# Optimization experiments

Measured on AMD Instinct MI355X. Metric: run time of the kernel, lower is better.

## Reference

```python
import jax, jax.numpy as jnp
import numpy as np

N, C, H, W = 8, 256, 64, 64
Q_REDUCE, K_REDUCE, V_REDUCE = 8, 8, 1


def setup_inputs() -> dict:
    key = jax.random.key(0)
    ks = jax.random.split(key, 6)
    Cq, Ck, Cv = C // Q_REDUCE, C // K_REDUCE, C // V_REDUCE
    s = 0.02
    x = jax.random.normal(ks[0], (N, C, H, W), dtype=jnp.float32)
    Wq = jax.random.normal(ks[1], (Cq, C), dtype=jnp.float32) * s
    Wk = jax.random.normal(ks[2], (Ck, C), dtype=jnp.float32) * s
    Wv = jax.random.normal(ks[3], (Cv, C), dtype=jnp.float32) * s
    Wo = jax.random.normal(ks[4], (C, Cv), dtype=jnp.float32) * s
    gamma = jax.random.normal(ks[5], (), dtype=jnp.float32)  # trained scalar (init 0.0 in torch)
    return {"x": x, "Wq": Wq, "Wk": Wk, "Wv": Wv, "Wo": Wo, "gamma": gamma}


def reference(x, Wq, Wk, Wv, Wo, gamma):
    n, c, h, w = x.shape
    xf = x.reshape(n, c, h * w)                      # [N, C, HW]
    q = jnp.einsum('qc,ncl->nql', Wq, xf)            # [N, Cq, HW] (1x1 conv)
    k = jnp.einsum('kc,ncl->nkl', Wk, xf)            # [N, Ck, HW]
    v = jnp.einsum('vc,ncl->nvl', Wv, xf)            # [N, Cv, HW]
    e = jnp.einsum('nci,ncj->nij', q, k)             # [N, HW, HW], unscaled energies
    a = jax.nn.softmax(e, axis=-1)                   # softmax over keys j
    o = jnp.einsum('nvi,nij->nvj', v, a)             # [N, Cv, HW]  (o = bmm(v, a))
    o = o.reshape(n, -1, w, h)                       # faithful: view(N,-1,W,H)
    out = jnp.einsum('ov,nvhw->nohw', Wo, o)         # output 1x1 conv
    return gamma * out
```

## Files before the change

### kernel.cpp

```cpp
#include <hip/hip_runtime.h>
#include <hip/hip_bf16.h>

#define NB 8
#define CIN 256
#define LL 4096
#define CQ 32
#define CV 256

typedef __attribute__((ext_vector_type(8))) short bf16x8;
typedef __attribute__((ext_vector_type(4))) float f32x4;

__device__ __forceinline__ unsigned short f2bf(float f) {
    union { __hip_bfloat16 h; unsigned short u; } c;
    c.h = __float2bfloat16(f);
    return c.u;
}
__device__ __forceinline__ unsigned int f2bf2(float a, float b) {
    union { __hip_bfloat162 h; unsigned int u; } c;
    float2 f; f.x = a; f.y = b;
    c.h = __float22bfloat162_rn(f);
    return c.u;
}

__global__ __launch_bounds__(256) void k_wcast(
    const float* __restrict__ Wq, const float* __restrict__ Wk,
    const float* __restrict__ Wv, const float* __restrict__ Wo,
    unsigned short* __restrict__ Wb, unsigned short* __restrict__ Wob)
{
    const float LOG2E = 1.4426950408889634f;
    const int row = blockIdx.x, t = threadIdx.x;
    if (row < 320) {
        float val;
        if (row < 32)      val = Wq[row * 256 + t] * LOG2E;
        else if (row < 64) val = Wk[(row - 32) * 256 + t];
        else               val = Wv[(row - 64) * 256 + t];
        Wb[row * 256 + t] = f2bf(val);
    } else {
        const int r2 = row - 320;
        Wob[r2 * 256 + t] = f2bf(Wo[r2 * 256 + t]);
    }
}

__global__ __launch_bounds__(512) void k_qkv3(
    const float* __restrict__ x, const unsigned short* __restrict__ Wb,
    unsigned short* __restrict__ qkt, unsigned short* __restrict__ v)
{
    __shared__ unsigned short xlds[64][264];
    __shared__ unsigned short tr[64][72];
    const int n = blockIdx.y, l0 = blockIdx.x * 64, t = threadIdx.x;
    const int w = t >> 6, lane = t & 63, lid = lane & 15, quad = lane >> 4;

    #pragma unroll
    for (int part = 0; part < 4; part++) {
        const int cbase = part * 64 + w * 8;
        float tmp[8];
        #pragma unroll
        for (int cc = 0; cc < 8; cc++)
            tmp[cc] = x[((size_t)n * CIN + cbase + cc) * LL + l0 + lane];
        bf16x8 s;
        #pragma unroll
        for (int cc = 0; cc < 8; cc++) s[cc] = (short)f2bf(tmp[cc]);
        *(bf16x8*)&xlds[lane][cbase] = s;
    }
    __syncthreads();

    const f32x4 fzero = {0.f, 0.f, 0.f, 0.f};
    f32x4 acc[3][4];
    #pragma unroll
    for (int mt = 0; mt < 3; mt++)
        #pragma unroll
        for (int nt = 0; nt < 4; nt++) acc[mt][nt] = fzero;

    for (int k0 = 0; k0 < 256; k0 += 32) {
        bf16x8 bx[4];
        #pragma unroll
        for (int nt = 0; nt < 4; nt++)
            bx[nt] = *(const bf16x8*)&xlds[nt * 16 + lid][k0 + quad * 8];
        #pragma unroll
        for (int vt = 0; vt < 2; vt++) {
            const bf16x8 wa = *(const bf16x8*)&Wb[(64 + w * 32 + vt * 16 + lid) * 256 + k0 + quad * 8];
            #pragma unroll
            for (int nt = 0; nt < 4; nt++)
                acc[vt][nt] = __builtin_amdgcn_mfma_f32_16x16x32_bf16(wa, bx[nt], acc[vt][nt], 0, 0, 0);
        }
        if (w < 4) {
            const bf16x8 wa = *(const bf16x8*)&Wb[(w * 16 + lid) * 256 + k0 + quad * 8];
            #pragma unroll
            for (int nt = 0; nt < 4; nt++)
                acc[2][nt] = __builtin_amdgcn_mfma_f32_16x16x32_bf16(wa, bx[nt], acc[2][nt], 0, 0, 0);
        }
    }
    #pragma unroll
    for (int vt = 0; vt < 2; vt++)
        #pragma unroll
        for (int nt = 0; nt < 4; nt++)
            #pragma unroll
            for (int reg = 0; reg < 4; reg++) {
                const int vr = w * 32 + vt * 16 + quad * 4 + reg;
                v[((size_t)n * CV + vr) * LL + l0 + nt * 16 + lid] = f2bf(acc[vt][nt][reg]);
            }
    if (w < 4) {
        #pragma unroll
        for (int nt = 0; nt < 4; nt++)
            #pragma unroll
            for (int reg = 0; reg < 4; reg++)
                tr[nt * 16 + lid][w * 16 + quad * 4 + reg] = f2bf(acc[2][nt][reg]);
    }
    __syncthreads();
    {
        const int l = t >> 3, c = (t & 7) * 8;
        *(uint4*)&qkt[((size_t)n * LL + l0 + l) * 64 + c] = *(const uint4*)&tr[l][c];
    }
}

__global__ __launch_bounds__(512) void k_rowsum3(
    const unsigned short* __restrict__ qkt, float* __restrict__ lns)
{
    __shared__ float red[64];
    const int n = blockIdx.y, i0 = blockIdx.x * 64, t = threadIdx.x;
    const int w = t >> 6, lid = t & 15, quad = (t & 63) >> 4;
    if (t < 64) red[t] = 0.f;
    __syncthreads();

    bf16x8 aq[4];
    #pragma unroll
    for (int mt = 0; mt < 4; mt++)
        aq[mt] = *(const bf16x8*)&qkt[((size_t)n * LL + i0 + mt * 16 + lid) * 64 + quad * 8];

    const f32x4 fzero = {0.f, 0.f, 0.f, 0.f};
    float sums[4][4];
    #pragma unroll
    for (int mt = 0; mt < 4; mt++)
        #pragma unroll
        for (int reg = 0; reg < 4; reg++) sums[mt][reg] = 0.f;

    for (int jt = 0; jt < 8; jt++) {
        const int j0 = jt * 512 + w * 64;
        bf16x8 bk[4];
        #pragma unroll
        for (int nt = 0; nt < 4; nt++)
            bk[nt] = *(const bf16x8*)&qkt[((size_t)n * LL + j0 + nt * 16 + lid) * 64 + 32 + quad * 8];
        #pragma unroll
        for (int mt = 0; mt < 4; mt++)
            #pragma unroll
            for (int nt = 0; nt < 4; nt++) {
                f32x4 e = __builtin_amdgcn_mfma_f32_16x16x32_bf16(aq[mt], bk[nt], fzero, 0, 0, 0);
                sums[mt][0] += __builtin_amdgcn_exp2f(e[0]);
                sums[mt][1] += __builtin_amdgcn_exp2f(e[1]);
                sums[mt][2] += __builtin_amdgcn_exp2f(e[2]);
                sums[mt][3] += __builtin_amdgcn_exp2f(e[3]);
            }
    }
    #pragma unroll
    for (int mt = 0; mt < 4; mt++)
        #pragma unroll
        for (int reg = 0; reg < 4; reg++) {
            float s = sums[mt][reg];
            s += __shfl_xor(s, 1); s += __shfl_xor(s, 2);
            s += __shfl_xor(s, 4); s += __shfl_xor(s, 8);
            if (lid == 0) atomicAdd(&red[mt * 16 + quad * 4 + reg], s);
        }
    __syncthreads();
    if (t < 64) lns[(size_t)n * LL + i0 + t] = -__builtin_log2f(red[t]);
}

__device__ __forceinline__ void write_p(unsigned short (*pl)[128], const f32x4* e,
                                        int w, int lid, int quad, int xkey)
{
    const int chunk = (2 * w + (quad >> 1)) ^ xkey;
    #pragma unroll
    for (int nt = 0; nt < 4; nt++) {
        uint2 d;
        d.x = f2bf2(__builtin_amdgcn_exp2f(e[nt][0]), __builtin_amdgcn_exp2f(e[nt][1]));
        d.y = f2bf2(__builtin_amdgcn_exp2f(e[nt][2]), __builtin_amdgcn_exp2f(e[nt][3]));
        *(uint2*)&pl[nt * 16 + lid][chunk * 8 + (quad & 1) * 4] = d;
    }
}

__global__ __launch_bounds__(512, 4) void k_attn6(
    const unsigned short* __restrict__ qkt, const unsigned short* __restrict__ v,
    const float* __restrict__ lns, const unsigned short* __restrict__ Wob,
    const float* __restrict__ gp, float* __restrict__ out)
{
    __shared__ unsigned short lraw[64 * 264];
    unsigned short (*plds)[64][128] = (unsigned short (*)[64][128])lraw;
    unsigned short (*olds)[264] = (unsigned short (*)[264])lraw;

    const int bid = blockIdx.x;
    const int n = bid & 7, j0 = (bid >> 3) * 64, t = threadIdx.x;
    const int w = t >> 6, lane = t & 63, lid = lane & 15, quad = lane >> 4;
    const int xkey = lid & 7;

    const unsigned short* qrow = qkt + ((size_t)n * LL + w * 16 + lid) * 64 + quad * 8;
    const float* lrow = lns + (size_t)n * LL + w * 16 + quad * 4;
    const unsigned short* vrow = v + ((size_t)n * CV + w * 32 + lid) * LL + quad * 8;

    bf16x8 bk[4];
    #pragma unroll
    for (int nt = 0; nt < 4; nt++)
        bk[nt] = *(const bf16x8*)&qkt[((size_t)n * LL + j0 + nt * 16 + lid) * 64 + 32 + quad * 8];

    const f32x4 fzero = {0.f, 0.f, 0.f, 0.f};
    f32x4 acc[2][4];
    #pragma unroll
    for (int mt = 0; mt < 2; mt++)
        #pragma unroll
        for (int nt = 0; nt < 4; nt++) acc[mt][nt] = fzero;

    bf16x8 aq = *(const bf16x8*)qrow;
    f32x4 lnsC = *(const f32x4*)lrow;
    {
        f32x4 e[4];
        #pragma unroll
        for (int nt = 0; nt < 4; nt++)
            e[nt] = __builtin_amdgcn_mfma_f32_16x16x32_bf16(aq, bk[nt], lnsC, 0, 0, 0);
        aq = *(const bf16x8*)(qrow + (size_t)128 * 64);
        lnsC = *(const f32x4*)(lrow + 128);
        write_p(plds[0], e, w, lid, quad, xkey);
    }
    bf16x8 av[8];
    #pragma unroll
    for (int mt = 0; mt < 2; mt++)
        #pragma unroll
        for (int h = 0; h < 4; h++)
            av[mt * 4 + h] = *(const bf16x8*)(vrow + (size_t)mt * 16 * LL + h * 32);
    __syncthreads();

    for (int ic = 0; ic < 31; ic++) {
        const int cur = ic & 1;
        const size_t i0 = (size_t)ic * 128;
        f32x4 e2[4];
        #pragma unroll
        for (int nt = 0; nt < 4; nt++)
            e2[nt] = __builtin_amdgcn_mfma_f32_16x16x32_bf16(aq, bk[nt], lnsC, 0, 0, 0);
        const size_t ipf = (ic < 30) ? (i0 + 256) : i0;
        aq = *(const bf16x8*)(qrow + ipf * 64);
        lnsC = *(const f32x4*)(lrow + ipf);
        write_p(plds[cur ^ 1], e2, w, lid, quad, xkey);
        #pragma unroll
        for (int h = 0; h < 4; h++) {
            bf16x8 bp[4];
            #pragma unroll
            for (int nt = 0; nt < 4; nt++)
                bp[nt] = *(const bf16x8*)&plds[cur][nt * 16 + lid][((4 * h + quad) ^ xkey) * 8];
            #pragma unroll
            for (int mt = 0; mt < 2; mt++)
                #pragma unroll
                for (int nt = 0; nt < 4; nt++)
                    acc[mt][nt] = __builtin_amdgcn_mfma_f32_16x16x32_bf16(av[mt * 4 + h], bp[nt], acc[mt][nt], 0, 0, 0);
            #pragma unroll
            for (int mt = 0; mt < 2; mt++)
                av[mt * 4 + h] = *(const bf16x8*)(vrow + (size_t)mt * 16 * LL + (i0 + 128) + h * 32);
        }
        __syncthreads();
    }
    #pragma unroll
    for (int h = 0; h < 4; h++) {
        bf16x8 bp[4];
        #pragma unroll
        for (int nt = 0; nt < 4; nt++)
            bp[nt] = *(const bf16x8*)&plds[1][nt * 16 + lid][((4 * h + quad) ^ xkey) * 8];
        #pragma unroll
        for (int mt = 0; mt < 2; mt++)
            #pragma unroll
            for (int nt = 0; nt < 4; nt++)
                acc[mt][nt] = __builtin_amdgcn_mfma_f32_16x16x32_bf16(av[mt * 4 + h], bp[nt], acc[mt][nt], 0, 0, 0);
    }
    __syncthreads();

    #pragma unroll
    for (int mt = 0; mt < 2; mt++)
        #pragma unroll
        for (int nt = 0; nt < 4; nt++) {
            ushort4 s;
            s.x = f2bf(acc[mt][nt][0]); s.y = f2bf(acc[mt][nt][1]);
            s.z = f2bf(acc[mt][nt][2]); s.w = f2bf(acc[mt][nt][3]);
            *(ushort4*)&olds[nt * 16 + lid][w * 32 + mt * 16 + quad * 4] = s;
        }
    __syncthreads();
    f32x4 oacc[2][4];
    #pragma unroll
    for (int mt = 0; mt < 2; mt++)
        #pragma unroll
        for (int nt = 0; nt < 4; nt++) oacc[mt][nt] = fzero;
    for (int k0 = 0; k0 < 256; k0 += 32) {
        bf16x8 bo[4];
        #pragma unroll
        for (int nt = 0; nt < 4; nt++)
            bo[nt] = *(const bf16x8*)&olds[nt * 16 + lid][k0 + quad * 8];
        #pragma unroll
        for (int mt = 0; mt < 2; mt++) {
            const bf16x8 wa = *(const bf16x8*)&Wob[(w * 32 + mt * 16 + lid) * 256 + k0 + quad * 8];
            #pragma unroll
            for (int nt = 0; nt < 4; nt++)
                oacc[mt][nt] = __builtin_amdgcn_mfma_f32_16x16x32_bf16(wa, bo[nt], oacc[mt][nt], 0, 0, 0);
        }
    }
    const float g = *gp;
    #pragma unroll
    for (int mt = 0; mt < 2; mt++)
        #pragma unroll
        for (int nt = 0; nt < 4; nt++)
            #pragma unroll
            for (int reg = 0; reg < 4; reg++) {
                const int r = w * 32 + mt * 16 + quad * 4 + reg;
                out[((size_t)n * CIN + r) * LL + j0 + nt * 16 + lid] = g * oacc[mt][nt][reg];
            }
}

extern "C" void kernel_launch(void* const* d_in, const int* in_sizes, int n_in,
                              void* d_out, int out_size, void* d_ws, size_t ws_size,
                              hipStream_t stream) {
    const float* x     = (const float*)d_in[0];
    const float* Wq    = (const float*)d_in[1];
    const float* Wk    = (const float*)d_in[2];
    const float* Wv    = (const float*)d_in[3];
    const float* Wo    = (const float*)d_in[4];
    const float* gamma = (const float*)d_in[5];

    unsigned short* qkt = (unsigned short*)d_ws;
    unsigned short* v   = qkt + (size_t)NB * LL * 64;
    unsigned short* Wb  = v + (size_t)NB * CV * LL;
    unsigned short* Wob = Wb + 320 * 256;
    float* lns          = (float*)(Wob + 256 * 256);
    float* out = (float*)d_out;

    k_wcast  <<<dim3(576),   256, 0, stream>>>(Wq, Wk, Wv, Wo, Wb, Wob);
    k_qkv3   <<<dim3(64, 8), 512, 0, stream>>>(x, Wb, qkt, v);
    k_rowsum3<<<dim3(64, 8), 512, 0, stream>>>(qkt, lns);
    k_attn6  <<<dim3(512),   512, 0, stream>>>(qkt, v, lns, Wob, gamma, out);
}
```

Baseline: 265.6 us.

## Split attention PV across two key-halves with wider per-wave channel tiles

Restructures the P·V stage so each wave owns 64 value channels (4 M-tiles) for half of each 128-key chunk, with two wave groups splitting keys and reducing partial outputs through shared memory at the end. The P tile is stored in a fragment-ready layout so each wave reads its B operand with a single contiguous load per lane instead of swizzled row reads. The intent is more MFMA reuse per P/V register load and less LDS traffic per MFMA. In exchange it raises accumulator register pressure (16 tiles instead of 8), adds a cross-group reduction that rounds the partial sum to bf16 before adding, and uses more shared memory.

```diff
diff --git a/kernel.cpp b/kernel.cpp
--- a/kernel.cpp
+++ b/kernel.cpp
@@ -15,11 +15,8 @@
     c.h = __float2bfloat16(f);
     return c.u;
 }
-__device__ __forceinline__ unsigned int f2bf2(float a, float b) {
-    union { __hip_bfloat162 h; unsigned int u; } c;
-    float2 f; f.x = a; f.y = b;
-    c.h = __float22bfloat162_rn(f);
-    return c.u;
+__device__ __forceinline__ float bf2f(unsigned short h) {
+    return __uint_as_float(((unsigned)h) << 16);
 }
 
 __global__ __launch_bounds__(256) void k_wcast(
@@ -164,36 +161,26 @@
     if (t < 64) lns[(size_t)n * LL + i0 + t] = -__builtin_log2f(red[t]);
 }
 
-__device__ __forceinline__ void write_p(unsigned short (*pl)[128], const f32x4* e,
-                                        int w, int lid, int quad, int xkey)
-{
-    const int chunk = (2 * w + (quad >> 1)) ^ xkey;
-    #pragma unroll
-    for (int nt = 0; nt < 4; nt++) {
-        uint2 d;
-        d.x = f2bf2(__builtin_amdgcn_exp2f(e[nt][0]), __builtin_amdgcn_exp2f(e[nt][1]));
-        d.y = f2bf2(__builtin_amdgcn_exp2f(e[nt][2]), __builtin_amdgcn_exp2f(e[nt][3]));
-        *(uint2*)&pl[nt * 16 + lid][chunk * 8 + (quad & 1) * 4] = d;
-    }
-}
-
-__global__ __launch_bounds__(512, 4) void k_attn6(
+__global__ __launch_bounds__(512, 4) void k_attn7(
     const unsigned short* __restrict__ qkt, const unsigned short* __restrict__ v,
     const float* __restrict__ lns, const unsigned short* __restrict__ Wob,
     const float* __restrict__ gp, float* __restrict__ out)
 {
-    __shared__ unsigned short lraw[64 * 264];
-    unsigned short (*plds)[64][128] = (unsigned short (*)[64][128])lraw;
-    unsigned short (*olds)[264] = (unsigned short (*)[264])lraw;
+    __shared__ unsigned short pbuf[2][4][4][64][8];
+    __shared__ unsigned short olds[64][264];
+    unsigned short* cbuf = &pbuf[0][0][0][0][0];
 
     const int bid = blockIdx.x;
     const int n = bid & 7, j0 = (bid >> 3) * 64, t = threadIdx.x;
     const int w = t >> 6, lane = t & 63, lid = lane & 15, quad = lane >> 4;
-    const int xkey = lid & 7;
+    const int g = w >> 2, wl = w & 3;
+    const int kbw = w >> 1;
+    const int qr = (w & 1) * 2 + (quad >> 1);
+    const int e0 = (quad & 1) * 4;
 
     const unsigned short* qrow = qkt + ((size_t)n * LL + w * 16 + lid) * 64 + quad * 8;
     const float* lrow = lns + (size_t)n * LL + w * 16 + quad * 4;
-    const unsigned short* vrow = v + ((size_t)n * CV + w * 32 + lid) * LL + quad * 8;
+    const unsigned short* vbase = v + ((size_t)n * CV + wl * 64 + lid) * LL + g * 64 + quad * 8;
 
     bf16x8 bk[4];
     #pragma unroll
@@ -201,9 +188,9 @@
         bk[nt] = *(const bf16x8*)&qkt[((size_t)n * LL + j0 + nt * 16 + lid) * 64 + 32 + quad * 8];
 
     const f32x4 fzero = {0.f, 0.f, 0.f, 0.f};
-    f32x4 acc[2][4];
-    #pragma unroll
-    for (int mt = 0; mt < 2; mt++)
+    f32x4 acc[4][4];
+    #pragma unroll
+    for (int mt = 0; mt < 4; mt++)
         #pragma unroll
         for (int nt = 0; nt < 4; nt++) acc[mt][nt] = fzero;
 
@@ -216,14 +203,20 @@
             e[nt] = __builtin_amdgcn_mfma_f32_16x16x32_bf16(aq, bk[nt], lnsC, 0, 0, 0);
         aq = *(const bf16x8*)(qrow + (size_t)128 * 64);
         lnsC = *(const f32x4*)(lrow + 128);
-        write_p(plds[0], e, w, lid, quad, xkey);
-    }
-    bf16x8 av[8];
-    #pragma unroll
-    for (int mt = 0; mt < 2; mt++)
-        #pragma unroll
-        for (int h = 0; h < 4; h++)
-            av[mt * 4 + h] = *(const bf16x8*)(vrow + (size_t)mt * 16 * LL + h * 32);
+        #pragma unroll
+        for (int nt = 0; nt < 4; nt++) {
+            ushort4 s;
+            s.x = f2bf(__builtin_amdgcn_exp2f(e[nt][0]));
+            s.y = f2bf(__builtin_amdgcn_exp2f(e[nt][1]));
+            s.z = f2bf(__builtin_amdgcn_exp2f(e[nt][2]));
+            s.w = f2bf(__builtin_amdgcn_exp2f(e[nt][3]));
+            *(ushort4*)&pbuf[0][nt][kbw][qr * 16 + lid][e0] = s;
+        }
+    }
+    bf16x8 av[4];
+    #pragma unroll
+    for (int mt = 0; mt < 4; mt++)
+        av[mt] = *(const bf16x8*)(vbase + (size_t)mt * 16 * LL);
     __syncthreads();
 
     for (int ic = 0; ic < 31; ic++) {
@@ -236,48 +229,103 @@
         const size_t ipf = (ic < 30) ? (i0 + 256) : i0;
         aq = *(const bf16x8*)(qrow + ipf * 64);
         lnsC = *(const f32x4*)(lrow + ipf);
-        write_p(plds[cur ^ 1], e2, w, lid, quad, xkey);
-        #pragma unroll
-        for (int h = 0; h < 4; h++) {
+        #pragma unroll
+        for (int nt = 0; nt < 4; nt++) {
+            ushort4 s;
+            s.x = f2bf(__builtin_amdgcn_exp2f(e2[nt][0]));
+            s.y = f2bf(__builtin_amdgcn_exp2f(e2[nt][1]));
+            s.z = f2bf(__builtin_amdgcn_exp2f(e2[nt][2]));
+            s.w = f2bf(__builtin_amdgcn_exp2f(e2[nt][3]));
+            *(ushort4*)&pbuf[cur ^ 1][nt][kbw][qr * 16 + lid][e0] = s;
+        }
+        {
             bf16x8 bp[4];
             #pragma unroll
             for (int nt = 0; nt < 4; nt++)
-                bp[nt] = *(const bf16x8*)&plds[cur][nt * 16 + lid][((4 * h + quad) ^ xkey) * 8];
-            #pragma unroll
-            for (int mt = 0; mt < 2; mt++)
+                bp[nt] = *(const bf16x8*)&pbuf[cur][nt][2 * g][lane][0];
+            #pragma unroll
+            for (int mt = 0; mt < 4; mt++)
                 #pragma unroll
                 for (int nt = 0; nt < 4; nt++)
-                    acc[mt][nt] = __builtin_amdgcn_mfma_f32_16x16x32_bf16(av[mt * 4 + h], bp[nt], acc[mt][nt], 0, 0, 0);
-            #pragma unroll
-            for (int mt = 0; mt < 2; mt++)
-                av[mt * 4 + h] = *(const bf16x8*)(vrow + (size_t)mt * 16 * LL + (i0 + 128) + h * 32);
+                    acc[mt][nt] = __builtin_amdgcn_mfma_f32_16x16x32_bf16(av[mt], bp[nt], acc[mt][nt], 0, 0, 0);
+            #pragma unroll
+            for (int mt = 0; mt < 4; mt++)
+                av[mt] = *(const bf16x8*)(vbase + (size_t)mt * 16 * LL + i0 + 32);
+        }
+        {
+            bf16x8 bp[4];
+            #pragma unroll
+            for (int nt = 0; nt < 4; nt++)
+                bp[nt] = *(const bf16x8*)&pbuf[cur][nt][2 * g + 1][lane][0];
+            #pragma unroll
+            for (int mt = 0; mt < 4; mt++)
+                #pragma unroll
+                for (int nt = 0; nt < 4; nt++)
+                    acc[mt][nt] = __builtin_amdgcn_mfma_f32_16x16x32_bf16(av[mt], bp[nt], acc[mt][nt], 0, 0, 0);
+            #pragma unroll
+            for (int mt = 0; mt < 4; mt++)
+                av[mt] = *(const bf16x8*)(vbase + (size_t)mt * 16 * LL + i0 + 128);
         }
         __syncthreads();
     }
-    #pragma unroll
-    for (int h = 0; h < 4; h++) {
-        bf16x8 bp[4];
-        #pragma unroll
-        for (int nt = 0; nt < 4; nt++)
-            bp[nt] = *(const bf16x8*)&plds[1][nt * 16 + lid][((4 * h + quad) ^ xkey) * 8];
-        #pragma unroll
-        for (int mt = 0; mt < 2; mt++)
-            #pragma unroll
-            for (int nt = 0; nt < 4; nt++)
-                acc[mt][nt] = __builtin_amdgcn_mfma_f32_16x16x32_bf16(av[mt * 4 + h], bp[nt], acc[mt][nt], 0, 0, 0);
-    }
-    __syncthreads();
-
-    #pragma unroll
-    for (int mt = 0; mt < 2; mt++)
-        #pragma unroll
-        for (int nt = 0; nt < 4; nt++) {
-            ushort4 s;
-            s.x = f2bf(acc[mt][nt][0]); s.y = f2bf(acc[mt][nt][1]);
-            s.z = f2bf(acc[mt][nt][2]); s.w = f2bf(acc[mt][nt][3]);
-            *(ushort4*)&olds[nt * 16 + lid][w * 32 + mt * 16 + quad * 4] = s;
-        }
-    __syncthreads();
+    {
+        const size_t i0 = (size_t)31 * 128;
+        {
+            bf16x8 bp[4];
+            #pragma unroll
+            for (int nt = 0; nt < 4; nt++)
+                bp[nt] = *(const bf16x8*)&pbuf[1][nt][2 * g][lane][0];
+            #pragma unroll
+            for (int mt = 0; mt < 4; mt++)
+                #pragma unroll
+                for (int nt = 0; nt < 4; nt++)
+                    acc[mt][nt] = __builtin_amdgcn_mfma_f32_16x16x32_bf16(av[mt], bp[nt], acc[mt][nt], 0, 0, 0);
+            #pragma unroll
+            for (int mt = 0; mt < 4; mt++)
+                av[mt] = *(const bf16x8*)(vbase + (size_t)mt * 16 * LL + i0 + 32);
+        }
+        {
+            bf16x8 bp[4];
+            #pragma unroll
+            for (int nt = 0; nt < 4; nt++)
+                bp[nt] = *(const bf16x8*)&pbuf[1][nt][2 * g + 1][lane][0];
+            #pragma unroll
+            for (int mt = 0; mt < 4; mt++)
+                #pragma unroll
+                for (int nt = 0; nt < 4; nt++)
+                    acc[mt][nt] = __builtin_amdgcn_mfma_f32_16x16x32_bf16(av[mt], bp[nt], acc[mt][nt], 0, 0, 0);
+        }
+    }
+    __syncthreads();
+
+    if (g == 1) {
+        #pragma unroll
+        for (int mt = 0; mt < 4; mt++)
+            #pragma unroll
+            for (int nt = 0; nt < 4; nt++) {
+                ushort4 s;
+                s.x = f2bf(acc[mt][nt][0]); s.y = f2bf(acc[mt][nt][1]);
+                s.z = f2bf(acc[mt][nt][2]); s.w = f2bf(acc[mt][nt][3]);
+                *(ushort4*)&cbuf[(((wl * 4 + mt) * 4 + nt) * 64 + lane) * 4] = s;
+            }
+    }
+    __syncthreads();
+    if (g == 0) {
+        #pragma unroll
+        for (int mt = 0; mt < 4; mt++)
+            #pragma unroll
+            for (int nt = 0; nt < 4; nt++) {
+                const ushort4 p = *(const ushort4*)&cbuf[(((wl * 4 + mt) * 4 + nt) * 64 + lane) * 4];
+                ushort4 s;
+                s.x = f2bf(acc[mt][nt][0] + bf2f(p.x));
+                s.y = f2bf(acc[mt][nt][1] + bf2f(p.y));
+                s.z = f2bf(acc[mt][nt][2] + bf2f(p.z));
+                s.w = f2bf(acc[mt][nt][3] + bf2f(p.w));
+                *(ushort4*)&olds[nt * 16 + lid][wl * 64 + mt * 16 + quad * 4] = s;
+            }
+    }
+    __syncthreads();
+
     f32x4 oacc[2][4];
     #pragma unroll
     for (int mt = 0; mt < 2; mt++)
@@ -296,7 +344,7 @@
                 oacc[mt][nt] = __builtin_amdgcn_mfma_f32_16x16x32_bf16(wa, bo[nt], oacc[mt][nt], 0, 0, 0);
         }
     }
-    const float g = *gp;
+    const float gm = *gp;
     #pragma unroll
     for (int mt = 0; mt < 2; mt++)
         #pragma unroll
@@ -304,7 +352,7 @@
             #pragma unroll
             for (int reg = 0; reg < 4; reg++) {
                 const int r = w * 32 + mt * 16 + quad * 4 + reg;
-                out[((size_t)n * CIN + r) * LL + j0 + nt * 16 + lid] = g * oacc[mt][nt][reg];
+                out[((size_t)n * CIN + r) * LL + j0 + nt * 16 + lid] = gm * oacc[mt][nt][reg];
             }
 }
 
@@ -328,5 +376,5 @@
     k_wcast  <<<dim3(576),   256, 0, stream>>>(Wq, Wk, Wv, Wo, Wb, Wob);
     k_qkv3   <<<dim3(64, 8), 512, 0, stream>>>(x, Wb, qkt, v);
     k_rowsum3<<<dim3(64, 8), 512, 0, stream>>>(qkt, lns);
-    k_attn6  <<<dim3(512),   512, 0, stream>>>(qkt, v, lns, Wob, gamma, out);
-}
+    k_attn7  <<<dim3(512),   512, 0, stream>>>(qkt, v, lns, Wob, gamma, out);
+}
```

New measurement: 283.5 us. 1.07x slower.
